# Optimization experiments

Measured on AMD Instinct MI355X. Metric: run time of the kernel, lower is better.

## Reference

```python
import jax, jax.numpy as jnp
import numpy as np

EPS = 1e-6

def layer_norm(x, g, b):
    m = jnp.mean(x, axis=-1, keepdims=True)
    v = jnp.mean(jnp.square(x - m), axis=-1, keepdims=True)
    return (x - m) * jax.lax.rsqrt(v + EPS) * g + b

def setup_inputs() -> dict:
    key = jax.random.key(0)
    ks = jax.random.split(key, 12)
    B, L, D, Dff, SK = 8, 4096, 512, 2048, 128
    s = 0.02
    return {
        "x": jax.random.normal(ks[0], (B, L, D), jnp.float32),
        "Wq": jax.random.normal(ks[1], (D, D), jnp.float32) * s,
        "bq": jnp.zeros((D,), jnp.float32),
        "Wk": jax.random.normal(ks[2], (D, D), jnp.float32) * s,
        "bk": jnp.zeros((D,), jnp.float32),
        "Wv": jax.random.normal(ks[3], (D, D), jnp.float32) * s,
        "bv": jnp.zeros((D,), jnp.float32),
        "Wo": jax.random.normal(ks[4], (D, D), jnp.float32) * s,
        "bo": jnp.zeros((D,), jnp.float32),
        "g1": jnp.ones((D,), jnp.float32),
        "b1": jnp.zeros((D,), jnp.float32),
        "W1f": jax.random.normal(ks[5], (D, Dff), jnp.float32) * s,
        "b1f": jnp.zeros((Dff,), jnp.float32),
        "W2f": jax.random.normal(ks[6], (Dff, D), jnp.float32) * s,
        "b2f": jnp.zeros((D,), jnp.float32),
        "g2": jnp.ones((D,), jnp.float32),
        "b2": jnp.zeros((D,), jnp.float32),
        "sample_idx": jax.random.randint(ks[7], (SK,), 0, L, jnp.int64),
    }

NUM_HEADS = 8
TOP_U = 128

def prob_sparse_attention(x, Wq, bq, Wk, bk, Wv, bv, Wo, bo, sample_idx):
    B, L, D = x.shape
    H = NUM_HEADS
    dh = D // H
    scale = 1.0 / jnp.sqrt(jnp.asarray(dh, x.dtype))
    # projections -> [B, H, L, dh]
    def split_heads(t):
        return t.reshape(B, L, H, dh).transpose(0, 2, 1, 3)
    Q = split_heads(x @ Wq + bq)
    K = split_heads(x @ Wk + bk)
    V = split_heads(x @ Wv + bv)
    # sparsity measurement on a sampled key subset: [B, H, L, SK]
    K_samp = K[:, :, sample_idx, :]
    s_samp = jnp.einsum('bhld,bhsd->bhls', Q, K_samp)
    M = jnp.max(s_samp, axis=-1) - jnp.mean(s_samp, axis=-1)  # [B, H, L]
    _, top_idx = jax.lax.top_k(M, TOP_U)  # [B, H, u]
    # gather top-u queries: [B, H, u, dh]
    Q_top = jnp.take_along_axis(Q, top_idx[..., None], axis=2)
    scores = jnp.einsum('bhud,bhld->bhul', Q_top, K) * scale  # [B, H, u, L]
    attn = jax.nn.softmax(scores, axis=-1)
    ctx_top = jnp.einsum('bhul,bhld->bhud', attn, V)  # [B, H, u, dh]
    # lazy queries get mean(V)
    meanV = jnp.mean(V, axis=2, keepdims=True)  # [B, H, 1, dh]
    ctx = jnp.broadcast_to(meanV, (B, H, L, dh))
    bi = jnp.arange(B)[:, None, None]
    hi = jnp.arange(H)[None, :, None]
    ctx = ctx.at[bi, hi, top_idx].set(ctx_top)
    out = ctx.transpose(0, 2, 1, 3).reshape(B, L, D)
    return out @ Wo + bo

def reference(x, Wq, bq, Wk, bk, Wv, bv, Wo, bo, g1, b1, W1f, b1f, W2f, b2f, g2, b2, sample_idx):
    attn_out = prob_sparse_attention(x, Wq, bq, Wk, bk, Wv, bv, Wo, bo, sample_idx)
    x1 = layer_norm(x + attn_out, g1, b1)
    ffn = jax.nn.relu(x1 @ W1f + b1f) @ W2f + b2f
    return layer_norm(x1 + ffn, g2, b2)
```

## Files before the change

### kernel.cpp

```cpp
#include <hip/hip_runtime.h>
#include <hip/hip_bf16.h>

using bf16 = __hip_bfloat16;

constexpr int Bd  = 8;
constexpr int Ld  = 4096;
constexpr int Dd  = 512;
constexpr int Hd  = 8;
constexpr int DHd = 64;
constexpr int DFFd= 2048;
constexpr int Ud  = 128;
constexpr int MLd = Bd * Ld;
constexpr int KSd = 16;

typedef short          bf16x8 __attribute__((ext_vector_type(8)));
typedef unsigned short u16x8  __attribute__((ext_vector_type(8)));
typedef float          f32x4  __attribute__((ext_vector_type(4)));

__device__ __forceinline__ float bf2float(bf16 v) { return __bfloat162float(v); }

__device__ __forceinline__ float wred_sum(float v) {
    #pragma unroll
    for (int o = 32; o > 0; o >>= 1) v += __shfl_xor(v, o);
    return v;
}
__device__ __forceinline__ float wred_max(float v) {
    #pragma unroll
    for (int o = 32; o > 0; o >>= 1) v = fmaxf(v, __shfl_xor(v, o));
    return v;
}
__device__ __forceinline__ float scrub(float v) {
    return (fabsf(v) < 1e20f) ? v : 0.0f;
}
__device__ __forceinline__ short f2bs(float f) {
    bf16 h = __float2bfloat16(f);
    return *reinterpret_cast<short*>(&h);
}

__device__ __forceinline__ void gload_lds16(const bf16* g, bf16* lds_base) {
    __builtin_amdgcn_global_load_lds((const __attribute__((address_space(1))) void*)g,
                                     (__attribute__((address_space(3))) void*)lds_base,
                                     16, 0, 0);
}

__global__ void detect_kernel(const void* xraw, int* flags) {
    const unsigned short* u = (const unsigned short*)xraw;
    __shared__ int cnt;
    if (threadIdx.x == 0) cnt = 0;
    __syncthreads();
    int local = 0;
    for (int i = threadIdx.x; i < 1024; i += 256) {
        int e = (u[2 * i] >> 7) & 0xFF;
        if (e >= 96 && e <= 142) local++;
    }
    atomicAdd(&cnt, local);
    __syncthreads();
    if (threadIdx.x == 0) flags[0] = (cnt < 512) ? 1 : 0;
}

__global__ void conv_kernel(const void* raw, bf16* dst, int n, const int* flags) {
    int i = blockIdx.x * 256 + threadIdx.x;
    if (i >= n) return;
    if (flags[0]) dst[i] = __float2bfloat16(((const float*)raw)[i]);
    else          dst[i] = ((const bf16*)raw)[i];
}

__global__ void convT_kernel(const void* raw, bf16* dst, int K, int N, const int* flags) {
    __shared__ bf16 tile[32][33];
    const int k0 = blockIdx.y * 32, n0 = blockIdx.x * 32;
    const int tx = threadIdx.x & 31, ty = threadIdx.x >> 5;
    #pragma unroll
    for (int p = 0; p < 4; ++p) {
        int k = k0 + ty + p * 8, n = n0 + tx;
        float v = flags[0] ? ((const float*)raw)[(size_t)k * N + n]
                           : bf2float(((const bf16*)raw)[(size_t)k * N + n]);
        tile[ty + p * 8][tx] = __float2bfloat16(v);
    }
    __syncthreads();
    #pragma unroll
    for (int p = 0; p < 4; ++p) {
        int n = n0 + ty + p * 8, k = k0 + tx;
        dst[(size_t)n * K + k] = tile[tx][ty + p * 8];
    }
}

__global__ void zero_kernel(int* p, int n) {
    int i = blockIdx.x * 256 + threadIdx.x;
    if (i < n) p[i] = 0;
}

__global__ void idx_kernel(const void* raw, int* out) {
    const int* r32 = (const int*)raw;
    __shared__ int is64;
    int t = threadIdx.x;
    if (t == 0) is64 = 1;
    __syncthreads();
    if (t < 64 && r32[2 * t + 1] != 0) is64 = 0;
    __syncthreads();
    int v = is64 ? r32[2 * t] : r32[t];
    out[t] = min(max(v, 0), Ld - 1);
}

template<bool RELU, bool QKV3>
__launch_bounds__(256)
__global__ void mfma_gemm(const bf16* __restrict__ X, const bf16* __restrict__ WT,
                          const bf16* __restrict__ bias, bf16* __restrict__ C,
                          int M, int N, int K)
{
    __shared__ bf16 As[2][128 * 64];
    __shared__ bf16 Bs[2][128 * 64];
    const int t = threadIdx.x;
    const int lane = t & 63, wave = t >> 6;
    const int wr = wave >> 1, wc = wave & 1;
    const int quad = lane >> 4, l15 = lane & 15;

    const int nwg = gridDim.x * gridDim.y;
    int wg = blockIdx.y * gridDim.x + blockIdx.x;
    if ((nwg & 7) == 0)
        wg = (wg & 7) * (nwg >> 3) + (wg >> 3);
    const int m0 = (wg / gridDim.x) * 128, n0 = (wg % gridDim.x) * 128;

    const int rseg = lane >> 3;
    const int cs   = (lane & 7) ^ rseg;

    auto stage = [&](int buf, int k0) {
        #pragma unroll
        for (int p = 0; p < 4; ++p) {
            const int sg = wave * 4 + p;
            const int r  = sg * 8 + rseg;
            gload_lds16(&X [(size_t)(m0 + r) * K + k0 + cs * 8], &As[buf][sg * 512]);
            gload_lds16(&WT[(size_t)(n0 + r) * K + k0 + cs * 8], &Bs[buf][sg * 512]);
        }
    };

    f32x4 acc[4][4] = {};

    stage(0, 0);
    __syncthreads();
    int cur = 0;
    const int NI = K >> 6;
    for (int it = 0; it < NI; ++it) {
        if (it + 1 < NI) stage(cur ^ 1, (it + 1) << 6);
        #pragma unroll
        for (int kk = 0; kk < 2; ++kk) {
            const int ch = ((kk * 4 + quad) ^ (l15 & 7)) * 8;
            bf16x8 a[4], b[4];
            #pragma unroll
            for (int i = 0; i < 4; ++i) {
                a[i] = *(const bf16x8*)&As[cur][(wr * 64 + i * 16 + l15) * 64 + ch];
                b[i] = *(const bf16x8*)&Bs[cur][(wc * 64 + i * 16 + l15) * 64 + ch];
            }
            #pragma unroll
            for (int i = 0; i < 4; ++i)
                #pragma unroll
                for (int j = 0; j < 4; ++j)
                    acc[i][j] = __builtin_amdgcn_mfma_f32_16x16x32_bf16(a[i], b[j], acc[i][j], 0, 0, 0);
        }
        if (it + 1 < NI) __syncthreads();
        cur ^= 1;
    }
    #pragma unroll
    for (int j = 0; j < 4; ++j) {
        int n = n0 + wc * 64 + j * 16 + l15;
        float bi = bf2float(bias[n]);
        bf16* cb;
        size_t stride;
        if (QKV3) {
            cb = C + (size_t)(n >> 9) * ((size_t)MLd * Dd) + (n & (Dd - 1));
            stride = Dd;
        } else {
            cb = C + n;
            stride = (size_t)N;
        }
        #pragma unroll
        for (int i = 0; i < 4; ++i) {
            #pragma unroll
            for (int r = 0; r < 4; ++r) {
                int m = m0 + wr * 64 + i * 16 + quad * 4 + r;
                float v = acc[i][j][r] + bi;
                if (RELU) v = fmaxf(v, 0.0f);
                cb[(size_t)m * stride] = __float2bfloat16(v);
            }
        }
    }
}

__launch_bounds__(256)
__global__ void m_kernel(const bf16* __restrict__ Q, const bf16* __restrict__ Kg,
                         const int* __restrict__ sidx, float* __restrict__ Mv)
{
    __shared__ __align__(16) short Qs[128 * 64];
    __shared__ __align__(16) short Ks[128 * 64];
    __shared__ int sidxs[128];

    const int t = threadIdx.x, lane = t & 63, w = t >> 6;
    const int l15 = lane & 15, quad = lane >> 4;
    const int l0 = blockIdx.x * 128;
    const int bh = blockIdx.y, b = bh >> 3, h = bh & 7;

    if (t < 128) sidxs[t] = sidx[t];
    __syncthreads();

    const int rseg = lane >> 3;
    const int cs   = (lane & 7) ^ rseg;
    #pragma unroll
    for (int sg4 = 0; sg4 < 4; ++sg4) {
        const int sg = w * 4 + sg4;
        const int r  = sg * 8 + rseg;
        gload_lds16(Q  + ((size_t)(b * Ld + l0 + r))    * Dd + h * 64 + cs * 8,
                    (bf16*)&Qs[sg * 512]);
        gload_lds16(Kg + ((size_t)(b * Ld + sidxs[r])) * Dd + h * 64 + cs * 8,
                    (bf16*)&Ks[sg * 512]);
    }
    __syncthreads();

    f32x4 s[2][8] = {};
    #pragma unroll
    for (int kk = 0; kk < 2; ++kk) {
        const int ch = ((kk * 4 + quad) ^ (l15 & 7)) * 8;
        bf16x8 qa[2], kb[8];
        #pragma unroll
        for (int mt = 0; mt < 2; ++mt)
            qa[mt] = *(const bf16x8*)&Qs[(w * 32 + mt * 16 + l15) * 64 + ch];
        #pragma unroll
        for (int nt = 0; nt < 8; ++nt)
            kb[nt] = *(const bf16x8*)&Ks[(nt * 16 + l15) * 64 + ch];
        #pragma unroll
        for (int mt = 0; mt < 2; ++mt)
            #pragma unroll
            for (int nt = 0; nt < 8; ++nt)
                s[mt][nt] = __builtin_amdgcn_mfma_f32_16x16x32_bf16(qa[mt], kb[nt], s[mt][nt], 0, 0, 0);
    }

    #pragma unroll
    for (int mt = 0; mt < 2; ++mt) {
        #pragma unroll
        for (int r = 0; r < 4; ++r) {
            float vmax = -1e30f, vsum = 0.0f;
            #pragma unroll
            for (int nt = 0; nt < 8; ++nt) {
                float v = s[mt][nt][r];
                vmax = fmaxf(vmax, v); vsum += v;
            }
            #pragma unroll
            for (int off = 1; off < 16; off <<= 1) {
                vmax = fmaxf(vmax, __shfl_xor(vmax, off));
                vsum += __shfl_xor(vsum, off);
            }
            if (l15 == 0) {
                const int row = w * 32 + mt * 16 + quad * 4 + r;
                Mv[(size_t)bh * Ld + l0 + row] = vmax - vsum * (1.0f / 128.0f);
            }
        }
    }
}

__launch_bounds__(256)
__global__ void topk_kernel(const float* __restrict__ Mv, int* __restrict__ topIdx)
{
    __shared__ unsigned ukey[4096];
    __shared__ short listA[4096], listB[4096];
    __shared__ int hist[256];
    __shared__ int outCnt, candCnt, selB, aboveK;
    const int bh = blockIdx.x, t = threadIdx.x;

    for (int i = t; i < 4096; i += 256) {
        unsigned u = __float_as_uint(Mv[(size_t)bh * Ld + i]);
        ukey[i] = (u & 0x80000000u) ? ~u : (u | 0x80000000u);
    }
    if (t == 0) outCnt = 0;
    __syncthreads();

    int K = Ud;
    #pragma unroll
    for (int r = 0; r < 4; ++r) {
        const int shift = 24 - 8 * r;
        hist[t] = 0;
        __syncthreads();
        const int n = (r == 0) ? 4096 : candCnt;
        const short* cur = (r & 1) ? listB : listA;
        for (int i = t; i < n; i += 256) {
            int idx = (r == 0) ? i : cur[i];
            atomicAdd(&hist[(ukey[idx] >> shift) & 0xFF], 1);
        }
        __syncthreads();
        if (t == 0) {
            int cum = 0, b = 255;
            for (; b > 0; --b) {
                if (cum + hist[b] >= K) break;
                cum += hist[b];
            }
            selB = b; aboveK = cum; candCnt = 0;
        }
        __syncthreads();
        const int sb = selB;
        short* nxt = (r & 1) ? listA : listB;
        for (int i = t; i < n; i += 256) {
            int idx = (r == 0) ? i : cur[i];
            int by = (ukey[idx] >> shift) & 0xFF;
            if (by > sb) {
                int p = atomicAdd(&outCnt, 1);
                topIdx[bh * Ud + p] = idx;
            } else if (by == sb) {
                int p = atomicAdd(&candCnt, 1);
                nxt[p] = (short)idx;
            }
        }
        __syncthreads();
        K -= aboveK;
        if (K == 0) break;
    }
    if (K > 0) {
        for (int i = t; i < K; i += 256) {
            int p = atomicAdd(&outCnt, 1);
            topIdx[bh * Ud + p] = listA[i];
        }
    }
}

__global__ void rows_kernel(const int* __restrict__ topIdx, int* __restrict__ rowCnt,
                            int* __restrict__ rowEnt)
{
    const int bh = blockIdx.x, u = threadIdx.x, b = bh >> 3;
    const int lq = topIdx[bh * Ud + u];
    const int row = b * Ld + lq;
    int slot = atomicAdd(&rowCnt[row], 1) & 7;
    rowEnt[row * 8 + slot] = bh * Ud + u;
}

__launch_bounds__(256)
__global__ void meanv_kernel(const bf16* __restrict__ V, float* __restrict__ meanV)
{
    const int bh = blockIdx.x, b = bh >> 3, h = bh & 7;
    const int l0 = blockIdx.y * 64;
    const int t = threadIdx.x;
    const int d = t & 63, part = t >> 6;
    float s = 0.0f;
    #pragma unroll
    for (int p = 0; p < 16; ++p) {
        int l = l0 + part + p * 4;
        s += bf2float(V[((size_t)(b * Ld + l)) * Dd + h * 64 + d]);
    }
    __shared__ float red[256];
    red[t] = s;
    __syncthreads();
    if (t < 64) {
        float tot = red[t] + red[64 + t] + red[128 + t] + red[192 + t];
        atomicAdd(&meanV[bh * 64 + t], tot * (1.0f / 4096.0f));
    }
}

__launch_bounds__(256, 3)
__global__ void attn_kernel(const bf16* __restrict__ Qg, const bf16* __restrict__ Kg,
                            const bf16* __restrict__ Vg, const int* __restrict__ topIdx,
                            bf16* __restrict__ pO, float* __restrict__ pM, float* __restrict__ pL)
{
    __shared__ __align__(16) short KsS[2][64 * 64];
    __shared__ __align__(16) short VsS[2][64 * 72];
    __shared__ __align__(16) short PsS[4][32 * 72];

    const int t = threadIdx.x, lane = t & 63, w = t >> 6;
    const int l15 = lane & 15, quad = lane >> 4;
    const int bh = blockIdx.x, ks = blockIdx.y;
    const int b = bh >> 3, h = bh & 7;
    const int key0 = ks * (Ld / KSd);
    constexpr int NT = (Ld / KSd) / 64;

    bf16x8 qf[2][2];
    #pragma unroll
    for (int m = 0; m < 2; ++m) {
        const int u  = w * 32 + m * 16 + l15;
        const int lq = topIdx[bh * Ud + u];
        const bf16* qr = Qg + ((size_t)(b * Ld + lq)) * Dd + h * 64;
        qf[m][0] = *(const bf16x8*)(qr + quad * 8);
        qf[m][1] = *(const bf16x8*)(qr + 32 + quad * 8);
    }

    const int vkey = t >> 2, vd0 = (t & 3) * 16;
    u16x8 vr0, vr1;

    auto loadV = [&](int tt) {
        const bf16* vs = Vg + ((size_t)(b * Ld + key0 + tt * 64 + vkey)) * Dd + h * 64 + vd0;
        vr0 = *(const u16x8*)vs;
        vr1 = *(const u16x8*)(vs + 8);
    };
    auto stageK = [&](int buf, int tt) {
        const int kb0 = key0 + tt * 64;
        #pragma unroll
        for (int sz = 0; sz < 2; ++sz) {
            const int sg = w * 2 + sz;
            const int r  = sg * 8 + (lane >> 3);
            const int cs = (lane & 7) ^ (lane >> 3);
            gload_lds16(Kg + ((size_t)(b * Ld + kb0 + r)) * Dd + h * 64 + cs * 8,
                        (bf16*)&KsS[buf][sg * 512]);
        }
    };
    auto writeV = [&](int buf) {
        #pragma unroll
        for (int j = 0; j < 8; ++j) {
            VsS[buf][(vd0 + j) * 72 + vkey]     = (short)vr0[j];
            VsS[buf][(vd0 + 8 + j) * 72 + vkey] = (short)vr1[j];
        }
    };

    float mrun[2][4], lrun[2][4];
    f32x4 o[2][4] = {};
    #pragma unroll
    for (int m = 0; m < 2; ++m)
        #pragma unroll
        for (int r = 0; r < 4; ++r) { mrun[m][r] = -1e30f; lrun[m][r] = 0.0f; }

    loadV(0); stageK(0, 0); writeV(0);
    __syncthreads();

    short* PsW = &PsS[w][0];
    for (int tt = 0; tt < NT; ++tt) {
        const int cur = tt & 1;
        if (tt + 1 < NT) { loadV(tt + 1); stageK(cur ^ 1, tt + 1); }

        const short* KsB = &KsS[cur][0];
        f32x4 s[2][4] = {};
        #pragma unroll
        for (int kk = 0; kk < 2; ++kk) {
            bf16x8 kb[4];
            #pragma unroll
            for (int n = 0; n < 4; ++n)
                kb[n] = *(const bf16x8*)&KsB[(n * 16 + l15) * 64 +
                                             (((kk * 4 + quad) ^ (l15 & 7)) * 8)];
            #pragma unroll
            for (int m = 0; m < 2; ++m)
                #pragma unroll
                for (int n = 0; n < 4; ++n)
                    s[m][n] = __builtin_amdgcn_mfma_f32_16x16x32_bf16(qf[m][kk], kb[n], s[m][n], 0, 0, 0);
        }

        #pragma unroll
        for (int m = 0; m < 2; ++m) {
            #pragma unroll
            for (int r = 0; r < 4; ++r) {
                float sv[4];
                #pragma unroll
                for (int n = 0; n < 4; ++n) sv[n] = s[m][n][r] * 0.125f;
                float vm = fmaxf(fmaxf(sv[0], sv[1]), fmaxf(sv[2], sv[3]));
                #pragma unroll
                for (int off = 1; off < 16; off <<= 1) vm = fmaxf(vm, __shfl_xor(vm, off));
                const float mn = fmaxf(mrun[m][r], vm);
                const float al = __expf(mrun[m][r] - mn);
                float ps = 0.0f;
                #pragma unroll
                for (int n = 0; n < 4; ++n) { sv[n] = __expf(sv[n] - mn); ps += sv[n]; }
                #pragma unroll
                for (int off = 1; off < 16; off <<= 1) ps += __shfl_xor(ps, off);
                lrun[m][r] = lrun[m][r] * al + ps;
                mrun[m][r] = mn;
                const int qrow = m * 16 + quad * 4 + r;
                #pragma unroll
                for (int n = 0; n < 4; ++n) {
                    PsW[qrow * 72 + n * 16 + l15] = f2bs(sv[n]);
                    o[m][n][r] *= al;
                }
            }
        }

        if (tt + 1 < NT) writeV(cur ^ 1);

        const short* VsB = &VsS[cur][0];
        #pragma unroll
        for (int kk = 0; kk < 2; ++kk) {
            bf16x8 pa[2], vb[4];
            #pragma unroll
            for (int m = 0; m < 2; ++m)
                pa[m] = *(const bf16x8*)&PsW[(m * 16 + l15) * 72 + kk * 32 + quad * 8];
            #pragma unroll
            for (int n = 0; n < 4; ++n)
                vb[n] = *(const bf16x8*)&VsB[(n * 16 + l15) * 72 + kk * 32 + quad * 8];
            #pragma unroll
            for (int m = 0; m < 2; ++m)
                #pragma unroll
                for (int n = 0; n < 4; ++n)
                    o[m][n] = __builtin_amdgcn_mfma_f32_16x16x32_bf16(pa[m], vb[n], o[m][n], 0, 0, 0);
        }
        __syncthreads();
    }

    const size_t pbase = ((size_t)(ks * 64 + bh)) * Ud;
    #pragma unroll
    for (int m = 0; m < 2; ++m) {
        #pragma unroll
        for (int r = 0; r < 4; ++r) {
            const int u = w * 32 + m * 16 + quad * 4 + r;
            #pragma unroll
            for (int n = 0; n < 4; ++n)
                pO[(pbase + u) * 64 + n * 16 + l15] = __float2bfloat16(o[m][n][r]);
            if (l15 == 0) { pM[pbase + u] = mrun[m][r]; pL[pbase + u] = lrun[m][r]; }
        }
    }
}

__launch_bounds__(256)
__global__ void combine_kernel(const bf16* __restrict__ pO, const float* __restrict__ pM,
                               const float* __restrict__ pL, float* __restrict__ ctxTop)
{
    const int t = threadIdx.x, c = t & 63, ui = t >> 6;
    const int u = (blockIdx.x & 31) * 4 + ui, bh = blockIdx.x >> 5;
    float mstar = -1e30f;
    #pragma unroll
    for (int ks = 0; ks < KSd; ++ks)
        mstar = fmaxf(mstar, pM[(ks * 64 + bh) * Ud + u]);
    float lsum = 0.0f, osum = 0.0f;
    #pragma unroll
    for (int ks = 0; ks < KSd; ++ks) {
        float wgt = __expf(pM[(ks * 64 + bh) * Ud + u] - mstar);
        lsum += pL[(ks * 64 + bh) * Ud + u] * wgt;
        osum += bf2float(pO[(((size_t)ks * 64 + bh) * Ud + u) * 64 + c]) * wgt;
    }
    ctxTop[((size_t)bh * Ud + u) * 64 + c] = scrub(osum / lsum);
}

__launch_bounds__(512)
__global__ void baseout_kernel(const float* __restrict__ meanV, const bf16* __restrict__ Wo,
                               const bf16* __restrict__ bo, float* __restrict__ baseOut)
{
    const int b = blockIdx.x, t = threadIdx.x;
    __shared__ float mv[512];
    mv[t] = meanV[b * 512 + t];
    __syncthreads();
    float acc = bf2float(bo[t]);
    for (int d = 0; d < 512; ++d)
        acc = fmaf(mv[d], bf2float(Wo[(size_t)d * 512 + t]), acc);
    baseOut[b * 512 + t] = acc;
}

__launch_bounds__(256)
__global__ void delta_kernel(const float* __restrict__ ctxTop, const float* __restrict__ meanV,
                             const bf16* __restrict__ Wo, bf16* __restrict__ deltaOut)
{
    const int u = blockIdx.x, bh = blockIdx.y, h = bh & 7, t = threadIdx.x;
    __shared__ float diff[64];
    if (t < 64) diff[t] = ctxTop[((size_t)bh * Ud + u) * 64 + t] - meanV[bh * 64 + t];
    __syncthreads();
    for (int n = t; n < 512; n += 256) {
        float acc = 0.0f;
        #pragma unroll 8
        for (int dd = 0; dd < 64; ++dd)
            acc = fmaf(diff[dd], bf2float(Wo[(size_t)(h * 64 + dd) * 512 + n]), acc);
        deltaOut[((size_t)bh * Ud + u) * 512 + n] = __float2bfloat16(acc);
    }
}

__launch_bounds__(256)
__global__ void ln1_kernel(const bf16* __restrict__ x, const float* __restrict__ baseOut,
                           const int* __restrict__ rowCnt, const int* __restrict__ rowEnt,
                           const bf16* __restrict__ deltaOut,
                           const bf16* __restrict__ g, const bf16* __restrict__ bb,
                           bf16* __restrict__ x1)
{
    const int row = blockIdx.x, t = threadIdx.x;
    const int b = row >> 12;
    const size_t base = (size_t)row * 512;
    float v0 = bf2float(x[base + t])       + baseOut[b * 512 + t];
    float v1 = bf2float(x[base + t + 256]) + baseOut[b * 512 + t + 256];
    const int cnt = min(rowCnt[row], 8);
    for (int e = 0; e < cnt; ++e) {
        const bf16* dr = &deltaOut[(size_t)rowEnt[row * 8 + e] * 512];
        v0 += bf2float(dr[t]);
        v1 += bf2float(dr[t + 256]);
    }
    v0 = scrub(v0); v1 = scrub(v1);
    float s = v0 + v1, q = v0 * v0 + v1 * v1;
    s = wred_sum(s); q = wred_sum(q);
    __shared__ float sred[4], qred[4];
    int lane = t & 63, w = t >> 6;
    if (lane == 0) { sred[w] = s; qred[w] = q; }
    __syncthreads();
    float tot  = sred[0] + sred[1] + sred[2] + sred[3];
    float totq = qred[0] + qred[1] + qred[2] + qred[3];
    float mean = tot * (1.0f / 512.0f);
    float var  = fmaxf(totq * (1.0f / 512.0f) - mean * mean, 0.0f);
    float rstd = rsqrtf(var + 1e-6f);
    x1[base + t]       = __float2bfloat16((v0 - mean) * rstd * bf2float(g[t])       + bf2float(bb[t]));
    x1[base + t + 256] = __float2bfloat16((v1 - mean) * rstd * bf2float(g[t + 256]) + bf2float(bb[t + 256]));
}

__launch_bounds__(256)
__global__ void ln2_kernel(const bf16* __restrict__ x1, const bf16* __restrict__ ffn,
                           const bf16* __restrict__ g, const bf16* __restrict__ bb,
                           void* __restrict__ out, const int* __restrict__ flags)
{
    const int row = blockIdx.x, t = threadIdx.x;
    const size_t base = (size_t)row * 512;
    float v0 = bf2float(x1[base + t])       + bf2float(ffn[base + t]);
    float v1 = bf2float(x1[base + t + 256]) + bf2float(ffn[base + t + 256]);
    v0 = scrub(v0); v1 = scrub(v1);
    float s = v0 + v1, q = v0 * v0 + v1 * v1;
    s = wred_sum(s); q = wred_sum(q);
    __shared__ float sred[4], qred[4];
    int lane = t & 63, w = t >> 6;
    if (lane == 0) { sred[w] = s; qred[w] = q; }
    __syncthreads();
    float tot  = sred[0] + sred[1] + sred[2] + sred[3];
    float totq = qred[0] + qred[1] + qred[2] + qred[3];
    float mean = tot * (1.0f / 512.0f);
    float var  = fmaxf(totq * (1.0f / 512.0f) - mean * mean, 0.0f);
    float rstd = rsqrtf(var + 1e-6f);
    float o0 = (v0 - mean) * rstd * bf2float(g[t])       + bf2float(bb[t]);
    float o1 = (v1 - mean) * rstd * bf2float(g[t + 256]) + bf2float(bb[t + 256]);
    if (flags[0]) {
        ((float*)out)[base + t]       = o0;
        ((float*)out)[base + t + 256] = o1;
    } else {
        ((bf16*)out)[base + t]       = __float2bfloat16(o0);
        ((bf16*)out)[base + t + 256] = __float2bfloat16(o1);
    }
}

extern "C" void kernel_launch(void* const* d_in, const int* in_sizes, int n_in,
                              void* d_out, int out_size, void* d_ws, size_t ws_size,
                              hipStream_t stream)
{
    const void* sraw = d_in[17];

    const size_t NQ = (size_t)MLd * Dd;
    char* w = (char*)d_ws;
    size_t off = 0;
    auto alloc = [&](size_t bytes) { void* p = w + off; off += (bytes + 63) & ~size_t(63); return p; };
    bf16*  Qb   = (bf16*)alloc(NQ * 2);
    bf16*  Kb   = (bf16*)alloc(NQ * 2);
    bf16*  Vb   = (bf16*)alloc(NQ * 2);
    bf16*  xc   = (bf16*)alloc(NQ * 2);
    bf16*  WTq  = (bf16*)alloc(Dd * Dd * 2);
    bf16*  WTk  = (bf16*)alloc(Dd * Dd * 2);
    bf16*  WTv  = (bf16*)alloc(Dd * Dd * 2);
    bf16*  Woc  = (bf16*)alloc(Dd * Dd * 2);
    bf16*  WT1f = (bf16*)alloc((size_t)Dd * DFFd * 2);
    bf16*  WT2f = (bf16*)alloc((size_t)DFFd * Dd * 2);
    bf16* bqc = (bf16*)alloc(Dd * 2);
    bf16* bkc = (bf16*)alloc(Dd * 2);
    bf16* bvc = (bf16*)alloc(Dd * 2);
    bf16* boc = (bf16*)alloc(Dd * 2);
    bf16* g1c = (bf16*)alloc(Dd * 2);
    bf16* b1c = (bf16*)alloc(Dd * 2);
    bf16* b1fc= (bf16*)alloc(DFFd * 2);
    bf16* b2fc= (bf16*)alloc(Dd * 2);
    bf16* g2c = (bf16*)alloc(Dd * 2);
    bf16* b2c = (bf16*)alloc(Dd * 2);
    bf16*  pOb     = (bf16*)alloc((size_t)KSd * 64 * Ud * 64 * 2);
    float* Mv      = (float*)alloc((size_t)Bd * Hd * Ld * 4);
    float* ctxTop  = (float*)alloc((size_t)Bd * Hd * Ud * DHd * 4);
    float* meanV   = (float*)alloc(Bd * Hd * DHd * 4);
    float* baseOut = (float*)alloc(Bd * Dd * 4);
    int*   topIdx  = (int*)alloc(Bd * Hd * Ud * 4);
    int*   sidx    = (int*)alloc(128 * 4);
    int*   rowCnt  = (int*)alloc(MLd * 4);
    int*   rowEnt  = (int*)alloc(MLd * 8 * 4);
    int*   flags   = (int*)alloc(64);
    if (off > ws_size) return;

    bf16* h1full = nullptr;
    if (ws_size - off >= (size_t)MLd * DFFd * 2 + 64)
        h1full = (bf16*)alloc((size_t)MLd * DFFd * 2);

    bf16*  x1b  = Vb;
    bf16*  h1b  = Qb;
    bf16*  ffnb = xc;
    bf16*  deltaOut = pOb;
    float* pM = Mv;
    float* pL = Mv + KSd * 64 * Ud;

    detect_kernel<<<1, 256, 0, stream>>>(d_in[0], flags);

    auto conv = [&](int i, bf16* dst, int n) {
        conv_kernel<<<(n + 255) / 256, 256, 0, stream>>>(d_in[i], dst, n, flags);
    };
    conv(0,  xc, (int)NQ);
    convT_kernel<<<dim3(Dd / 32, Dd / 32), 256, 0, stream>>>(d_in[1], WTq, Dd, Dd, flags);
    convT_kernel<<<dim3(Dd / 32, Dd / 32), 256, 0, stream>>>(d_in[3], WTk, Dd, Dd, flags);
    convT_kernel<<<dim3(Dd / 32, Dd / 32), 256, 0, stream>>>(d_in[5], WTv, Dd, Dd, flags);
    convT_kernel<<<dim3(DFFd / 32, Dd / 32), 256, 0, stream>>>(d_in[11], WT1f, Dd, DFFd, flags);
    convT_kernel<<<dim3(Dd / 32, DFFd / 32), 256, 0, stream>>>(d_in[13], WT2f, DFFd, Dd, flags);
    conv(7,  Woc, Dd * Dd);
    conv(2,  bqc, Dd);  conv(4,  bkc, Dd);  conv(6,  bvc, Dd);  conv(8,  boc, Dd);
    conv(9,  g1c, Dd);  conv(10, b1c, Dd);
    conv(12, b1fc, DFFd); conv(14, b2fc, Dd);
    conv(15, g2c, Dd);  conv(16, b2c, Dd);

    zero_kernel<<<(MLd + 255) / 256, 256, 0, stream>>>(rowCnt, MLd);
    zero_kernel<<<(Bd * Hd * DHd + 255) / 256, 256, 0, stream>>>((int*)meanV, Bd * Hd * DHd);
    idx_kernel<<<1, 128, 0, stream>>>(sraw, sidx);

    mfma_gemm<false, true><<<dim3(12, 256), 256, 0, stream>>>(xc, WTq, bqc, Qb, MLd, 3 * Dd, Dd);

    m_kernel<<<dim3(Ld / 128, Bd * Hd), 256, 0, stream>>>(Qb, Kb, sidx, Mv);
    topk_kernel<<<Bd * Hd, 256, 0, stream>>>(Mv, topIdx);
    rows_kernel<<<Bd * Hd, 128, 0, stream>>>(topIdx, rowCnt, rowEnt);
    meanv_kernel<<<dim3(Bd * Hd, Ld / 64), 256, 0, stream>>>(Vb, meanV);

    attn_kernel<<<dim3(Bd * Hd, KSd), 256, 0, stream>>>(Qb, Kb, Vb, topIdx, pOb, pM, pL);
    combine_kernel<<<Bd * Hd * 32, 256, 0, stream>>>(pOb, pM, pL, ctxTop);

    baseout_kernel<<<Bd, 512, 0, stream>>>(meanV, Woc, boc, baseOut);
    delta_kernel<<<dim3(Ud, Bd * Hd), 256, 0, stream>>>(ctxTop, meanV, Woc, deltaOut);

    ln1_kernel<<<MLd, 256, 0, stream>>>(xc, baseOut, rowCnt, rowEnt, deltaOut, g1c, b1c, x1b);

    if (h1full) {
        mfma_gemm<true , false><<<dim3(16, 256), 256, 0, stream>>>(x1b, WT1f, b1fc, h1full, MLd, DFFd, Dd);
        mfma_gemm<false, false><<<dim3(4, 256), 256, 0, stream>>>(h1full, WT2f, b2fc, ffnb, MLd, Dd, DFFd);
    } else {
        for (int c = 0; c < 2; ++c) {
            mfma_gemm<true , false><<<dim3(16, 128), 256, 0, stream>>>(
                x1b + (size_t)c * 16384 * 512, WT1f, b1fc, h1b, 16384, DFFd, Dd);
            mfma_gemm<false, false><<<dim3(4, 128), 256, 0, stream>>>(
                h1b, WT2f, b2fc, ffnb + (size_t)c * 16384 * 512, 16384, Dd, DFFd);
        }
    }

    ln2_kernel<<<MLd, 256, 0, stream>>>(x1b, ffnb, g2c, b2c, d_out, flags);
}
```

Measured before the change: 669.0 us.

## Fuse delta projection into LN1, batch small conversions, parallelize baseout

After: 658.5 us. About the same (-1.6%).

```diff
diff --git a/kernel.cpp b/kernel.cpp
--- a/kernel.cpp
+++ b/kernel.cpp
@@ -24,11 +24,6 @@
     for (int o = 32; o > 0; o >>= 1) v += __shfl_xor(v, o);
     return v;
 }
-__device__ __forceinline__ float wred_max(float v) {
-    #pragma unroll
-    for (int o = 32; o > 0; o >>= 1) v = fmaxf(v, __shfl_xor(v, o));
-    return v;
-}
 __device__ __forceinline__ float scrub(float v) {
     return (fabsf(v) < 1e20f) ? v : 0.0f;
 }
@@ -63,6 +58,26 @@
     if (i >= n) return;
     if (flags[0]) dst[i] = __float2bfloat16(((const float*)raw)[i]);
     else          dst[i] = ((const bf16*)raw)[i];
+}
+
+struct ConvBatch {
+    const void* src[12];
+    void*       dst[12];
+    int         n[12];
+    int         mode[12];
+};
+__global__ void conv_batch_kernel(ConvBatch cb, const int* __restrict__ flags) {
+    const int d = blockIdx.x, n = cb.n[d];
+    if (cb.mode[d] == 1) {
+        int* p = (int*)cb.dst[d];
+        for (int i = threadIdx.x; i < n; i += 256) p[i] = 0;
+    } else {
+        bf16* p = (bf16*)cb.dst[d];
+        for (int i = threadIdx.x; i < n; i += 256) {
+            if (flags[0]) p[i] = __float2bfloat16(((const float*)cb.src[d])[i]);
+            else          p[i] = ((const bf16*)cb.src[d])[i];
+        }
+    }
 }
 
 __global__ void convT_kernel(const void* raw, bf16* dst, int K, int N, const int* flags) {
@@ -517,41 +532,30 @@
     ctxTop[((size_t)bh * Ud + u) * 64 + c] = scrub(osum / lsum);
 }
 
-__launch_bounds__(512)
+__launch_bounds__(256)
 __global__ void baseout_kernel(const float* __restrict__ meanV, const bf16* __restrict__ Wo,
                                const bf16* __restrict__ bo, float* __restrict__ baseOut)
 {
     const int b = blockIdx.x, t = threadIdx.x;
+    const int n = blockIdx.y * 128 + (t >> 1), half = t & 1;
     __shared__ float mv[512];
     mv[t] = meanV[b * 512 + t];
-    __syncthreads();
-    float acc = bf2float(bo[t]);
-    for (int d = 0; d < 512; ++d)
-        acc = fmaf(mv[d], bf2float(Wo[(size_t)d * 512 + t]), acc);
-    baseOut[b * 512 + t] = acc;
-}
-
-__launch_bounds__(256)
-__global__ void delta_kernel(const float* __restrict__ ctxTop, const float* __restrict__ meanV,
-                             const bf16* __restrict__ Wo, bf16* __restrict__ deltaOut)
-{
-    const int u = blockIdx.x, bh = blockIdx.y, h = bh & 7, t = threadIdx.x;
-    __shared__ float diff[64];
-    if (t < 64) diff[t] = ctxTop[((size_t)bh * Ud + u) * 64 + t] - meanV[bh * 64 + t];
-    __syncthreads();
-    for (int n = t; n < 512; n += 256) {
-        float acc = 0.0f;
-        #pragma unroll 8
-        for (int dd = 0; dd < 64; ++dd)
-            acc = fmaf(diff[dd], bf2float(Wo[(size_t)(h * 64 + dd) * 512 + n]), acc);
-        deltaOut[((size_t)bh * Ud + u) * 512 + n] = __float2bfloat16(acc);
-    }
+    mv[t + 256] = meanV[b * 512 + t + 256];
+    __syncthreads();
+    float acc = 0.0f;
+    const int d0 = half * 256;
+    #pragma unroll 8
+    for (int d = 0; d < 256; ++d)
+        acc = fmaf(mv[d0 + d], bf2float(Wo[(size_t)(d0 + d) * 512 + n]), acc);
+    acc += __shfl_xor(acc, 1);
+    if (half == 0) baseOut[b * 512 + n] = acc + bf2float(bo[n]);
 }
 
 __launch_bounds__(256)
 __global__ void ln1_kernel(const bf16* __restrict__ x, const float* __restrict__ baseOut,
                            const int* __restrict__ rowCnt, const int* __restrict__ rowEnt,
-                           const bf16* __restrict__ deltaOut,
+                           const float* __restrict__ ctxTop, const float* __restrict__ meanV,
+                           const bf16* __restrict__ Wo,
                            const bf16* __restrict__ g, const bf16* __restrict__ bb,
                            bf16* __restrict__ x1)
 {
@@ -561,10 +565,22 @@
     float v0 = bf2float(x[base + t])       + baseOut[b * 512 + t];
     float v1 = bf2float(x[base + t + 256]) + baseOut[b * 512 + t + 256];
     const int cnt = min(rowCnt[row], 8);
+    __shared__ float diff[64];
     for (int e = 0; e < cnt; ++e) {
-        const bf16* dr = &deltaOut[(size_t)rowEnt[row * 8 + e] * 512];
-        v0 += bf2float(dr[t]);
-        v1 += bf2float(dr[t + 256]);
+        const int bhu = rowEnt[row * 8 + e];
+        const int bh = bhu >> 7, u = bhu & 127, h = bh & 7;
+        if (t < 64) diff[t] = ctxTop[((size_t)bh * Ud + u) * 64 + t] - meanV[bh * 64 + t];
+        __syncthreads();
+        float a0 = 0.0f, a1 = 0.0f;
+        #pragma unroll 8
+        for (int dd = 0; dd < 64; ++dd) {
+            const float df = diff[dd];
+            const bf16* wr = Wo + (size_t)(h * 64 + dd) * 512;
+            a0 = fmaf(df, bf2float(wr[t]), a0);
+            a1 = fmaf(df, bf2float(wr[t + 256]), a1);
+        }
+        v0 += a0; v1 += a1;
+        __syncthreads();
     }
     v0 = scrub(v0); v1 = scrub(v1);
     float s = v0 + v1, q = v0 * v0 + v1 * v1;
@@ -663,29 +679,31 @@
     bf16*  x1b  = Vb;
     bf16*  h1b  = Qb;
     bf16*  ffnb = xc;
-    bf16*  deltaOut = pOb;
     float* pM = Mv;
     float* pL = Mv + KSd * 64 * Ud;
 
     detect_kernel<<<1, 256, 0, stream>>>(d_in[0], flags);
 
-    auto conv = [&](int i, bf16* dst, int n) {
-        conv_kernel<<<(n + 255) / 256, 256, 0, stream>>>(d_in[i], dst, n, flags);
-    };
-    conv(0,  xc, (int)NQ);
+    conv_kernel<<<((int)NQ + 255) / 256, 256, 0, stream>>>(d_in[0], xc, (int)NQ, flags);
     convT_kernel<<<dim3(Dd / 32, Dd / 32), 256, 0, stream>>>(d_in[1], WTq, Dd, Dd, flags);
     convT_kernel<<<dim3(Dd / 32, Dd / 32), 256, 0, stream>>>(d_in[3], WTk, Dd, Dd, flags);
     convT_kernel<<<dim3(Dd / 32, Dd / 32), 256, 0, stream>>>(d_in[5], WTv, Dd, Dd, flags);
     convT_kernel<<<dim3(DFFd / 32, Dd / 32), 256, 0, stream>>>(d_in[11], WT1f, Dd, DFFd, flags);
     convT_kernel<<<dim3(Dd / 32, DFFd / 32), 256, 0, stream>>>(d_in[13], WT2f, DFFd, Dd, flags);
-    conv(7,  Woc, Dd * Dd);
-    conv(2,  bqc, Dd);  conv(4,  bkc, Dd);  conv(6,  bvc, Dd);  conv(8,  boc, Dd);
-    conv(9,  g1c, Dd);  conv(10, b1c, Dd);
-    conv(12, b1fc, DFFd); conv(14, b2fc, Dd);
-    conv(15, g2c, Dd);  conv(16, b2c, Dd);
+    conv_kernel<<<(Dd * Dd + 255) / 256, 256, 0, stream>>>(d_in[7], Woc, Dd * Dd, flags);
+
+    ConvBatch cb;
+    const int srcIdx[10] = {2, 4, 6, 8, 9, 10, 12, 14, 15, 16};
+    bf16* dsts[10] = {bqc, bkc, bvc, boc, g1c, b1c, b1fc, b2fc, g2c, b2c};
+    for (int i = 0; i < 10; ++i) {
+        cb.src[i] = d_in[srcIdx[i]]; cb.dst[i] = dsts[i];
+        cb.n[i] = (i == 6) ? DFFd : Dd; cb.mode[i] = 0;
+    }
+    cb.src[10] = nullptr; cb.dst[10] = meanV; cb.n[10] = Bd * Hd * DHd; cb.mode[10] = 1;
+    cb.src[11] = nullptr; cb.dst[11] = flags; cb.n[11] = 0; cb.mode[11] = 1;
+    conv_batch_kernel<<<11, 256, 0, stream>>>(cb, flags);
 
     zero_kernel<<<(MLd + 255) / 256, 256, 0, stream>>>(rowCnt, MLd);
-    zero_kernel<<<(Bd * Hd * DHd + 255) / 256, 256, 0, stream>>>((int*)meanV, Bd * Hd * DHd);
     idx_kernel<<<1, 128, 0, stream>>>(sraw, sidx);
 
     mfma_gemm<false, true><<<dim3(12, 256), 256, 0, stream>>>(xc, WTq, bqc, Qb, MLd, 3 * Dd, Dd);
@@ -698,10 +716,10 @@
     attn_kernel<<<dim3(Bd * Hd, KSd), 256, 0, stream>>>(Qb, Kb, Vb, topIdx, pOb, pM, pL);
     combine_kernel<<<Bd * Hd * 32, 256, 0, stream>>>(pOb, pM, pL, ctxTop);
 
-    baseout_kernel<<<Bd, 512, 0, stream>>>(meanV, Woc, boc, baseOut);
-    delta_kernel<<<dim3(Ud, Bd * Hd), 256, 0, stream>>>(ctxTop, meanV, Woc, deltaOut);
-
-    ln1_kernel<<<MLd, 256, 0, stream>>>(xc, baseOut, rowCnt, rowEnt, deltaOut, g1c, b1c, x1b);
+    baseout_kernel<<<dim3(Bd, 4), 256, 0, stream>>>(meanV, Woc, boc, baseOut);
+
+    ln1_kernel<<<MLd, 256, 0, stream>>>(xc, baseOut, rowCnt, rowEnt,
+                                        ctxTop, meanV, Woc, g1c, b1c, x1b);
 
     if (h1full) {
         mfma_gemm<true , false><<<dim3(16, 256), 256, 0, stream>>>(x1b, WT1f, b1fc, h1full, MLd, DFFd, Dd);
```
